# Kernel tuning notes

Measured on AMD Instinct MI355X. Metric: run time of the kernel, lower is better.

## Reference

```python
import jax, jax.numpy as jnp
import numpy as np

NUM_SCALES = 4
ENC = 64
KMAX = 16
DT = 0.005  # base_time_constant; original code's (undefined) self.dt interpreted as this


def setup_inputs() -> dict:
    key = jax.random.key(0)
    ks = jax.random.split(key, 5)
    events = jax.random.normal(ks[0], (2, 2, 32, 32, 64), dtype=jnp.float32)
    # matches torch.logspace(-3, -1, num_scales)
    time_constants = jnp.logspace(-3.0, -1.0, NUM_SCALES).astype(jnp.float32)
    temporal_kernels = jax.random.normal(ks[1], (NUM_SCALES, ENC, KMAX), dtype=jnp.float32)
    w1 = jax.random.normal(ks[2], (2 * NUM_SCALES, NUM_SCALES), dtype=jnp.float32) * 0.1
    b1 = jnp.zeros((2 * NUM_SCALES,), dtype=jnp.float32)
    w2 = jax.random.normal(ks[3], (NUM_SCALES, 2 * NUM_SCALES), dtype=jnp.float32) * 0.1
    b2 = jnp.zeros((NUM_SCALES,), dtype=jnp.float32)
    return {"events": events, "time_constants": time_constants,
            "temporal_kernels": temporal_kernels, "w1": w1, "b1": b1, "w2": w2, "b2": b2}


def reference(events, time_constants, temporal_kernels, w1, b1, w2, b2):
    B, C, H, W, T = events.shape
    k = min(KMAX, T)
    # decay kernels per scale: [S, k], normalized to sum 1
    t_idx = jnp.arange(k, dtype=jnp.float32)
    decay = jnp.exp(-t_idx[None, :] * DT / time_constants[:, None])
    decay = decay / decay.sum(axis=-1, keepdims=True)
    # combined learnable kernels: [S, E, k]
    combined = decay[:, None, :] * temporal_kernels[:, :, :k]

    Cf = C * H * W
    # one batched cross-correlation (torch F.conv1d semantics == lax conv, no flip)
    x = events.reshape(B * Cf, 1, T)                       # [B*Cf, 1, T]
    kern = combined.reshape(NUM_SCALES * ENC, 1, k)        # [S*E, 1, k]
    out = jax.lax.conv_general_dilated(
        x, kern, window_strides=(1,), padding=[(k // 2, k // 2)],
        dimension_numbers=("NCH", "OIH", "NCH"))           # [B*Cf, S*E, T+1]
    Tp = out.shape[-1]
    # [B, E, S, Cf, Tp] matching torch stack order (enc at dim1, scale at dim2)
    feats = out.reshape(B, Cf, NUM_SCALES, ENC, Tp).transpose(0, 3, 2, 1, 4)

    # torch .var() is unbiased -> ddof=1
    feature_variance = feats.var(axis=-1, ddof=1).mean(axis=(1, 3))  # [B, S]
    h = jax.nn.relu(feature_variance @ w1.T + b1)
    attn = jax.nn.softmax(h @ w2.T + b2, axis=-1)                    # [B, S]

    encoded = (feats * attn[:, None, :, None, None]).sum(axis=2)     # [B, E, Cf, Tp]
    return encoded
```

## Files before the change

kernel.cpp:

```cpp
#include <hip/hip_runtime.h>

#define KK 16
#define SS 4
#define EE 64
#define BB 2
#define DT_CONST 0.005f

typedef float f32x4 __attribute__((ext_vector_type(4)));
typedef short bf16x8 __attribute__((ext_vector_type(8)));

#define WS_WK_F 34816

__global__ void __launch_bounds__(512, 1) kA_gram(const float* __restrict__ events,
                                                  float* __restrict__ ws) {
    __shared__ float xs[16][97];
    __shared__ float S1L[16][16];
    __shared__ float part[16][136];
    const int tid = threadIdx.x;

    if (tid < 256) {
        const float4* src = reinterpret_cast<const float4*>(
            events + (size_t)blockIdx.x * 1024);
        float4 v = src[tid];
        int r = tid >> 4, c0 = ((tid & 15) << 2) + 8;
        xs[r][c0] = v.x; xs[r][c0+1] = v.y; xs[r][c0+2] = v.z; xs[r][c0+3] = v.w;
    }
    for (int idx = tid; idx < 16 * 33; idx += 512) {
        int rr = idx / 33, k = idx % 33;
        xs[rr][(k < 8) ? k : (k + 64)] = 0.f;
    }
    __syncthreads();

    const int r   = tid >> 5;
    const int c   = tid & 31;
    const int lag = c >> 1;
    const int h   = c & 1;
    const int off = h * 33;
    const float inv65 = 1.f / 65.f;

    {
        float s = 0.f;
#pragma unroll
        for (int j = 0; j < 32; ++j) s += xs[r][lag + off + j];
        if (!h) s += xs[r][lag + 32];
        s += __shfl_xor(s, 1, 64);
        if (!h) S1L[r][lag] = s;
    }
    __syncthreads();

    {
        float C = 0.f;
#pragma unroll
        for (int j = 0; j < 32; ++j) C += xs[r][off + j] * xs[r][off + j + lag];
        if (!h) C += xs[r][32] * xs[r][32 + lag];
        {
            float Ct = C + __shfl_xor(C, 1, 64);
            if (!h) part[r][lag] = Ct - S1L[r][0] * S1L[r][lag] * inv65;
        }
#pragma unroll
        for (int d1 = 1; d1 <= 15; ++d1) {
            const int add = d1 + off + 32 - h;
            const int rem = d1 - 1 + off;
            C += xs[r][add] * xs[r][add + lag] - xs[r][rem] * xs[r][rem + lag];
            if (lag + d1 <= 15) {
                float Ct = C + __shfl_xor(C, 1, 64);
                if (!h) {
                    int p = 16 * d1 - ((d1 * (d1 - 1)) >> 1) + lag;
                    part[r][p] = Ct - S1L[r][d1] * S1L[r][d1 + lag] * inv65;
                }
            } else {
            }
        }
    }
    __syncthreads();

    if (tid < 136) {
        float g = 0.f;
#pragma unroll
        for (int rr = 0; rr < 16; ++rr) g += part[rr][tid];
        ws[((size_t)((blockIdx.x >> 7) * 136 + tid)) * 128 + (blockIdx.x & 127)] = g;
    }
}

__global__ void __launch_bounds__(256, 1) kM_mlp(const float* __restrict__ tc,
        const float* __restrict__ tk, const float* __restrict__ w1,
        const float* __restrict__ b1, const float* __restrict__ w2,
        const float* __restrict__ b2, float* __restrict__ ws) {
    __shared__ float Gf[2 * 256];
    __shared__ float combL[SS * EE * KK];
    __shared__ float fvL[BB * SS];
    __shared__ float attnL[BB][SS];
    const int tid = threadIdx.x;

    for (int v = tid; v < 272; v += 256) {
        int b = (v >= 136) ? 1 : 0;
        int p = v - b * 136;
        int pp = p, d1 = 0;
        while (pp >= KK - d1) { pp -= KK - d1; ++d1; }
        int d2 = d1 + pp;
        const float4* rp = reinterpret_cast<const float4*>(ws + (size_t)v * 128);
        float acc = 0.f;
#pragma unroll
        for (int i = 0; i < 32; ++i) { float4 q = rp[i]; acc += (q.x + q.y) + (q.z + q.w); }
        Gf[b * 256 + d1 * KK + d2] = acc;
        Gf[b * 256 + d2 * KK + d1] = acc;
    }
    {
        int s = tid >> 6;
        float inv = DT_CONST / tc[s];
        float dk[KK]; float dsum = 0.f;
#pragma unroll
        for (int j = 0; j < KK; ++j) { dk[j] = expf(-(float)j * inv); dsum += dk[j]; }
        float rn = 1.f / dsum;
#pragma unroll
        for (int i = 0; i < 4; ++i) {
            float4 v = reinterpret_cast<const float4*>(tk + tid * KK)[i];
            combL[tid * KK + 4*i + 0] = dk[4*i + 0] * rn * v.x;
            combL[tid * KK + 4*i + 1] = dk[4*i + 1] * rn * v.y;
            combL[tid * KK + 4*i + 2] = dk[4*i + 2] * rn * v.z;
            combL[tid * KK + 4*i + 3] = dk[4*i + 3] * rn * v.w;
        }
    }
    __syncthreads();
    {
        float cvec[KK];
#pragma unroll
        for (int i = 0; i < 4; ++i) {
            float4 v = reinterpret_cast<const float4*>(combL + tid * KK)[i];
            cvec[4*i] = v.x; cvec[4*i+1] = v.y; cvec[4*i+2] = v.z; cvec[4*i+3] = v.w;
        }
        float acc0 = 0.f, acc1 = 0.f;
#pragma unroll
        for (int d1 = 0; d1 < KK; ++d1) {
            float cd1 = cvec[d1];
            float t0 = 0.5f * Gf[d1 * KK + d1] * cd1;
            float t1 = 0.5f * Gf[256 + d1 * KK + d1] * cd1;
#pragma unroll
            for (int d2 = d1 + 1; d2 < KK; ++d2) {
                t0 += Gf[d1 * KK + d2] * cvec[d2];
                t1 += Gf[256 + d1 * KK + d2] * cvec[d2];
            }
            acc0 += 2.f * cd1 * t0;
            acc1 += 2.f * cd1 * t1;
        }
#pragma unroll
        for (int sft = 1; sft < 64; sft <<= 1) {
            acc0 += __shfl_xor(acc0, sft, 64);
            acc1 += __shfl_xor(acc1, sft, 64);
        }
        if ((tid & 63) == 0) {
            const float scale = 1.f / 8388608.f;
            fvL[(tid >> 6)]     = acc0 * scale;
            fvL[4 + (tid >> 6)] = acc1 * scale;
        }
    }
    __syncthreads();
    if (tid < 2) {
        int b = tid;
        float h[8];
#pragma unroll
        for (int i = 0; i < 8; ++i) {
            float a = b1[i];
#pragma unroll
            for (int s = 0; s < SS; ++s) a += fvL[b * SS + s] * w1[i * SS + s];
            h[i] = a > 0.f ? a : 0.f;
        }
        float lg[SS]; float mx = -1e30f;
#pragma unroll
        for (int s = 0; s < SS; ++s) {
            float a = b2[s];
#pragma unroll
            for (int i = 0; i < 8; ++i) a += h[i] * w2[s * 8 + i];
            lg[s] = a; mx = fmaxf(mx, a);
        }
        float se = 0.f;
#pragma unroll
        for (int s = 0; s < SS; ++s) { lg[s] = expf(lg[s] - mx); se += lg[s]; }
#pragma unroll
        for (int s = 0; s < SS; ++s) attnL[b][s] = lg[s] / se;
    }
    __syncthreads();
    {
        unsigned short* wkp = reinterpret_cast<unsigned short*>(ws + WS_WK_F);
#pragma unroll
        for (int j = 0; j < 8; ++j) {
            int o = tid * 8 + j;
            int b = o >> 10, e = (o >> 4) & 63, k = o & 15;
            float a = 0.f;
#pragma unroll
            for (int s = 0; s < SS; ++s)
                a += attnL[b][s] * combL[(s * EE + e) * KK + k];
            unsigned int bits = __float_as_uint(a);
            unsigned short hh = (unsigned short)(bits >> 16);
            float hf = __uint_as_float(((unsigned int)hh) << 16);
            unsigned short ll = (unsigned short)(__float_as_uint(a - hf) >> 16);
            int base = b * 2048 + e * 32 + k;
            wkp[base]          = hh;   wkp[base + 16]        = 0;
            wkp[4096 + base]   = ll;   wkp[4096 + base + 16] = 0;
        }
    }
}

__global__ void __launch_bounds__(256, 8) kC_conv(const float* __restrict__ events,
                                                  const float* __restrict__ ws,
                                                  float* __restrict__ out) {
    __shared__ float xs[2][97];
    __shared__ __align__(16) unsigned short Bh[80 * 24 + 16];
    __shared__ __align__(16) unsigned short Bl[80 * 24 + 16];
    const int tid = threadIdx.x;
    const int bid = blockIdx.x;
    const int b   = bid >> 10;
    const int cf0 = (bid & 1023) << 1;
    const int w   = tid >> 6, l = tid & 63, llo = l & 15, lhi = l >> 4;

    for (int idx = tid; idx < 80 * 24 + 16; idx += 256) { Bh[idx] = 0; Bl[idx] = 0; }

    const unsigned short* wkp = reinterpret_cast<const unsigned short*>(ws + WS_WK_F);
    bf16x8 Ah = *reinterpret_cast<const bf16x8*>(wkp + b * 2048 + (w * 16 + llo) * 32 + 8 * lhi);
    bf16x8 Al = *reinterpret_cast<const bf16x8*>(wkp + 4096 + b * 2048 + (w * 16 + llo) * 32 + 8 * lhi);

    if (tid < 32) {
        float4 v = reinterpret_cast<const float4*>(
            events + ((size_t)b * 2048 + cf0) * 64)[tid];
        int rr = tid >> 4, c0 = ((tid & 15) << 2) + 8;
        xs[rr][c0] = v.x; xs[rr][c0+1] = v.y; xs[rr][c0+2] = v.z; xs[rr][c0+3] = v.w;
    }
    for (int idx = tid; idx < 66; idx += 256) {
        int rr = idx / 33, k = idx % 33;
        xs[rr][(k < 8) ? k : (k + 64)] = 0.f;
    }
    __syncthreads();

#pragma unroll 1
    for (int rr = 0; rr < 2; ++rr) {
#pragma unroll
        for (int q = 0; q < 5; ++q) {
            int idx = tid + q * 256;
            int t = idx >> 4, k = idx & 15;
            float x = xs[rr][t + k];
            unsigned int bits = __float_as_uint(x);
            unsigned short hh = (unsigned short)(bits >> 16);
            float hf = __uint_as_float(((unsigned int)hh) << 16);
            unsigned short ll = (unsigned short)(__float_as_uint(x - hf) >> 16);
            Bh[t * 24 + k] = hh;
            Bl[t * 24 + k] = ll;
        }
        __syncthreads();

        const size_t obase = ((size_t)(b * 64 + w * 16 + lhi * 4) * 2048 + (cf0 + rr)) * 65;
#pragma unroll
        for (int nt = 0; nt < 5; ++nt) {
            bf16x8 Xh = *reinterpret_cast<const bf16x8*>(Bh + (nt * 16 + llo) * 24 + 8 * lhi);
            bf16x8 Xl = *reinterpret_cast<const bf16x8*>(Bl + (nt * 16 + llo) * 24 + 8 * lhi);
            f32x4 acc = {0.f, 0.f, 0.f, 0.f};
            acc = __builtin_amdgcn_mfma_f32_16x16x32_bf16(Al, Xh, acc, 0, 0, 0);
            acc = __builtin_amdgcn_mfma_f32_16x16x32_bf16(Ah, Xl, acc, 0, 0, 0);
            acc = __builtin_amdgcn_mfma_f32_16x16x32_bf16(Ah, Xh, acc, 0, 0, 0);
            const int t0 = nt * 16 + llo;
            if (t0 < 65) {
#pragma unroll
                for (int i = 0; i < 4; ++i)
                    out[obase + (size_t)i * (2048 * 65) + t0] = acc[i];
            }
        }
        __syncthreads();
    }
}

extern "C" void kernel_launch(void* const* d_in, const int* in_sizes, int n_in,
                              void* d_out, int out_size, void* d_ws, size_t ws_size,
                              hipStream_t stream) {
    const float* events = (const float*)d_in[0];
    const float* tc     = (const float*)d_in[1];
    const float* tk     = (const float*)d_in[2];
    const float* w1     = (const float*)d_in[3];
    const float* b1     = (const float*)d_in[4];
    const float* w2     = (const float*)d_in[5];
    const float* b2     = (const float*)d_in[6];
    float* out = (float*)d_out;
    float* ws  = (float*)d_ws;

    hipLaunchKernelGGL(kA_gram, dim3(256),  dim3(512), 0, stream, events, ws);
    hipLaunchKernelGGL(kM_mlp,  dim3(1),    dim3(256), 0, stream, tc, tk, w1, b1, w2, b2, ws);
    hipLaunchKernelGGL(kC_conv, dim3(2048), dim3(256), 0, stream, events, ws, out);
}
```

Measured before the change: 37.95 us.

## Fuse attention MLP into conv kernel and reduce Gram partials with atomics

New measurement: 43.81 us. 1.15x slower.

```diff
diff --git a/kernel.cpp b/kernel.cpp
--- a/kernel.cpp
+++ b/kernel.cpp
@@ -9,7 +9,6 @@
 typedef float f32x4 __attribute__((ext_vector_type(4)));
 typedef short bf16x8 __attribute__((ext_vector_type(8)));
 
-#define WS_WK_F 34816
 
 __global__ void __launch_bounds__(512, 1) kA_gram(const float* __restrict__ events,
                                                   float* __restrict__ ws) {
@@ -68,7 +67,6 @@
                     int p = 16 * d1 - ((d1 * (d1 - 1)) >> 1) + lag;
                     part[r][p] = Ct - S1L[r][d1] * S1L[r][d1 + lag] * inv65;
                 }
-            } else {
             }
         }
     }
@@ -78,133 +76,22 @@
         float g = 0.f;
 #pragma unroll
         for (int rr = 0; rr < 16; ++rr) g += part[rr][tid];
-        ws[((size_t)((blockIdx.x >> 7) * 136 + tid)) * 128 + (blockIdx.x & 127)] = g;
+        atomicAdd(&ws[(blockIdx.x >> 7) * 136 + tid], g);
     }
 }
 
-__global__ void __launch_bounds__(256, 1) kM_mlp(const float* __restrict__ tc,
+__global__ void __launch_bounds__(256, 8) kC_conv(
+        const float* __restrict__ events, const float* __restrict__ tc,
         const float* __restrict__ tk, const float* __restrict__ w1,
         const float* __restrict__ b1, const float* __restrict__ w2,
-        const float* __restrict__ b2, float* __restrict__ ws) {
+        const float* __restrict__ b2, const float* __restrict__ ws,
+        float* __restrict__ out) {
+    __shared__ float xs[2][97];
     __shared__ float Gf[2 * 256];
-    __shared__ float combL[SS * EE * KK];
+    __shared__ float decayL[SS * KK];
     __shared__ float fvL[BB * SS];
-    __shared__ float attnL[BB][SS];
-    const int tid = threadIdx.x;
-
-    for (int v = tid; v < 272; v += 256) {
-        int b = (v >= 136) ? 1 : 0;
-        int p = v - b * 136;
-        int pp = p, d1 = 0;
-        while (pp >= KK - d1) { pp -= KK - d1; ++d1; }
-        int d2 = d1 + pp;
-        const float4* rp = reinterpret_cast<const float4*>(ws + (size_t)v * 128);
-        float acc = 0.f;
-#pragma unroll
-        for (int i = 0; i < 32; ++i) { float4 q = rp[i]; acc += (q.x + q.y) + (q.z + q.w); }
-        Gf[b * 256 + d1 * KK + d2] = acc;
-        Gf[b * 256 + d2 * KK + d1] = acc;
-    }
-    {
-        int s = tid >> 6;
-        float inv = DT_CONST / tc[s];
-        float dk[KK]; float dsum = 0.f;
-#pragma unroll
-        for (int j = 0; j < KK; ++j) { dk[j] = expf(-(float)j * inv); dsum += dk[j]; }
-        float rn = 1.f / dsum;
-#pragma unroll
-        for (int i = 0; i < 4; ++i) {
-            float4 v = reinterpret_cast<const float4*>(tk + tid * KK)[i];
-            combL[tid * KK + 4*i + 0] = dk[4*i + 0] * rn * v.x;
-            combL[tid * KK + 4*i + 1] = dk[4*i + 1] * rn * v.y;
-            combL[tid * KK + 4*i + 2] = dk[4*i + 2] * rn * v.z;
-            combL[tid * KK + 4*i + 3] = dk[4*i + 3] * rn * v.w;
-        }
-    }
-    __syncthreads();
-    {
-        float cvec[KK];
-#pragma unroll
-        for (int i = 0; i < 4; ++i) {
-            float4 v = reinterpret_cast<const float4*>(combL + tid * KK)[i];
-            cvec[4*i] = v.x; cvec[4*i+1] = v.y; cvec[4*i+2] = v.z; cvec[4*i+3] = v.w;
-        }
-        float acc0 = 0.f, acc1 = 0.f;
-#pragma unroll
-        for (int d1 = 0; d1 < KK; ++d1) {
-            float cd1 = cvec[d1];
-            float t0 = 0.5f * Gf[d1 * KK + d1] * cd1;
-            float t1 = 0.5f * Gf[256 + d1 * KK + d1] * cd1;
-#pragma unroll
-            for (int d2 = d1 + 1; d2 < KK; ++d2) {
-                t0 += Gf[d1 * KK + d2] * cvec[d2];
-                t1 += Gf[256 + d1 * KK + d2] * cvec[d2];
-            }
-            acc0 += 2.f * cd1 * t0;
-            acc1 += 2.f * cd1 * t1;
-        }
-#pragma unroll
-        for (int sft = 1; sft < 64; sft <<= 1) {
-            acc0 += __shfl_xor(acc0, sft, 64);
-            acc1 += __shfl_xor(acc1, sft, 64);
-        }
-        if ((tid & 63) == 0) {
-            const float scale = 1.f / 8388608.f;
-            fvL[(tid >> 6)]     = acc0 * scale;
-            fvL[4 + (tid >> 6)] = acc1 * scale;
-        }
-    }
-    __syncthreads();
-    if (tid < 2) {
-        int b = tid;
-        float h[8];
-#pragma unroll
-        for (int i = 0; i < 8; ++i) {
-            float a = b1[i];
-#pragma unroll
-            for (int s = 0; s < SS; ++s) a += fvL[b * SS + s] * w1[i * SS + s];
-            h[i] = a > 0.f ? a : 0.f;
-        }
-        float lg[SS]; float mx = -1e30f;
-#pragma unroll
-        for (int s = 0; s < SS; ++s) {
-            float a = b2[s];
-#pragma unroll
-            for (int i = 0; i < 8; ++i) a += h[i] * w2[s * 8 + i];
-            lg[s] = a; mx = fmaxf(mx, a);
-        }
-        float se = 0.f;
-#pragma unroll
-        for (int s = 0; s < SS; ++s) { lg[s] = expf(lg[s] - mx); se += lg[s]; }
-#pragma unroll
-        for (int s = 0; s < SS; ++s) attnL[b][s] = lg[s] / se;
-    }
-    __syncthreads();
-    {
-        unsigned short* wkp = reinterpret_cast<unsigned short*>(ws + WS_WK_F);
-#pragma unroll
-        for (int j = 0; j < 8; ++j) {
-            int o = tid * 8 + j;
-            int b = o >> 10, e = (o >> 4) & 63, k = o & 15;
-            float a = 0.f;
-#pragma unroll
-            for (int s = 0; s < SS; ++s)
-                a += attnL[b][s] * combL[(s * EE + e) * KK + k];
-            unsigned int bits = __float_as_uint(a);
-            unsigned short hh = (unsigned short)(bits >> 16);
-            float hf = __uint_as_float(((unsigned int)hh) << 16);
-            unsigned short ll = (unsigned short)(__float_as_uint(a - hf) >> 16);
-            int base = b * 2048 + e * 32 + k;
-            wkp[base]          = hh;   wkp[base + 16]        = 0;
-            wkp[4096 + base]   = ll;   wkp[4096 + base + 16] = 0;
-        }
-    }
-}
-
-__global__ void __launch_bounds__(256, 8) kC_conv(const float* __restrict__ events,
-                                                  const float* __restrict__ ws,
-                                                  float* __restrict__ out) {
-    __shared__ float xs[2][97];
+    __shared__ __align__(16) unsigned short wkh[64 * 32];
+    __shared__ __align__(16) unsigned short wkl[64 * 32];
     __shared__ __align__(16) unsigned short Bh[80 * 24 + 16];
     __shared__ __align__(16) unsigned short Bl[80 * 24 + 16];
     const int tid = threadIdx.x;
@@ -213,12 +100,8 @@
     const int cf0 = (bid & 1023) << 1;
     const int w   = tid >> 6, l = tid & 63, llo = l & 15, lhi = l >> 4;
 
+    for (int idx = tid; idx < 2048; idx += 256) { wkh[idx] = 0; wkl[idx] = 0; }
     for (int idx = tid; idx < 80 * 24 + 16; idx += 256) { Bh[idx] = 0; Bl[idx] = 0; }
-
-    const unsigned short* wkp = reinterpret_cast<const unsigned short*>(ws + WS_WK_F);
-    bf16x8 Ah = *reinterpret_cast<const bf16x8*>(wkp + b * 2048 + (w * 16 + llo) * 32 + 8 * lhi);
-    bf16x8 Al = *reinterpret_cast<const bf16x8*>(wkp + 4096 + b * 2048 + (w * 16 + llo) * 32 + 8 * lhi);
-
     if (tid < 32) {
         float4 v = reinterpret_cast<const float4*>(
             events + ((size_t)b * 2048 + cf0) * 64)[tid];
@@ -229,7 +112,120 @@
         int rr = idx / 33, k = idx % 33;
         xs[rr][(k < 8) ? k : (k + 64)] = 0.f;
     }
-    __syncthreads();
+    for (int v = tid; v < 272; v += 256) {
+        int b2i = (v >= 136) ? 1 : 0;
+        int p  = v - b2i * 136;
+        int pp = p, d1 = 0;
+        while (pp >= KK - d1) { pp -= KK - d1; ++d1; }
+        int d2 = d1 + pp;
+        float g = ws[v];
+        Gf[b2i * 256 + d1 * KK + d2] = g;
+        Gf[b2i * 256 + d2 * KK + d1] = g;
+    }
+    if (tid < SS) {
+        float inv = DT_CONST / tc[tid];
+        float d[KK]; float sum = 0.f;
+#pragma unroll
+        for (int k = 0; k < KK; ++k) { d[k] = expf(-(float)k * inv); sum += d[k]; }
+        float rn = 1.f / sum;
+#pragma unroll
+        for (int k = 0; k < KK; ++k) decayL[tid * KK + k] = d[k] * rn;
+    }
+    __syncthreads();
+
+    {
+        const int s = tid >> 6, e = tid & 63;
+        const float4* tkr = reinterpret_cast<const float4*>(tk + (s * EE + e) * KK);
+        float cvec[KK];
+#pragma unroll
+        for (int i = 0; i < 4; ++i) {
+            float4 v = tkr[i];
+            cvec[4*i+0] = decayL[s * KK + 4*i+0] * v.x;
+            cvec[4*i+1] = decayL[s * KK + 4*i+1] * v.y;
+            cvec[4*i+2] = decayL[s * KK + 4*i+2] * v.z;
+            cvec[4*i+3] = decayL[s * KK + 4*i+3] * v.w;
+        }
+        float acc0 = 0.f, acc1 = 0.f;
+#pragma unroll
+        for (int d1 = 0; d1 < KK; ++d1) {
+            float cd1 = cvec[d1];
+            float t0 = 0.5f * Gf[d1 * KK + d1] * cd1;
+            float t1 = 0.5f * Gf[256 + d1 * KK + d1] * cd1;
+#pragma unroll
+            for (int d2 = d1 + 1; d2 < KK; ++d2) {
+                t0 += Gf[d1 * KK + d2] * cvec[d2];
+                t1 += Gf[256 + d1 * KK + d2] * cvec[d2];
+            }
+            acc0 += 2.f * cd1 * t0;
+            acc1 += 2.f * cd1 * t1;
+        }
+#pragma unroll
+        for (int sft = 1; sft < 64; sft <<= 1) {
+            acc0 += __shfl_xor(acc0, sft, 64);
+            acc1 += __shfl_xor(acc1, sft, 64);
+        }
+        if ((tid & 63) == 0) {
+            const float scale = 1.f / 8388608.f;
+            fvL[s]     = acc0 * scale;
+            fvL[4 + s] = acc1 * scale;
+        }
+    }
+    __syncthreads();
+
+    {
+        float fv[SS];
+#pragma unroll
+        for (int s = 0; s < SS; ++s) fv[s] = fvL[b * SS + s];
+        float h[8];
+#pragma unroll
+        for (int i = 0; i < 8; ++i) {
+            float a = b1[i];
+#pragma unroll
+            for (int s = 0; s < SS; ++s) a += fv[s] * w1[i * SS + s];
+            h[i] = a > 0.f ? a : 0.f;
+        }
+        float lg[SS]; float mx = -1e30f;
+#pragma unroll
+        for (int s = 0; s < SS; ++s) {
+            float a = b2[s];
+#pragma unroll
+            for (int i = 0; i < 8; ++i) a += h[i] * w2[s * 8 + i];
+            lg[s] = a; mx = fmaxf(mx, a);
+        }
+        float se = 0.f;
+#pragma unroll
+        for (int s = 0; s < SS; ++s) { lg[s] = expf(lg[s] - mx); se += lg[s]; }
+        float attn[SS];
+#pragma unroll
+        for (int s = 0; s < SS; ++s) attn[s] = lg[s] / se;
+
+        const int o4 = tid * 4;
+        const int e  = o4 >> 4, k0 = o4 & 15;
+        float vj0 = 0.f, vj1 = 0.f, vj2 = 0.f, vj3 = 0.f;
+#pragma unroll
+        for (int s = 0; s < SS; ++s) {
+            float4 tv = *reinterpret_cast<const float4*>(tk + (s * EE + e) * KK + k0);
+            float as = attn[s];
+            vj0 += as * decayL[s * KK + k0 + 0] * tv.x;
+            vj1 += as * decayL[s * KK + k0 + 1] * tv.y;
+            vj2 += as * decayL[s * KK + k0 + 2] * tv.z;
+            vj3 += as * decayL[s * KK + k0 + 3] * tv.w;
+        }
+        float vv[4] = {vj0, vj1, vj2, vj3};
+#pragma unroll
+        for (int j = 0; j < 4; ++j) {
+            unsigned int bits = __float_as_uint(vv[j]);
+            unsigned short hh = (unsigned short)(bits >> 16);
+            float hf = __uint_as_float(((unsigned int)hh) << 16);
+            unsigned short ll = (unsigned short)(__float_as_uint(vv[j] - hf) >> 16);
+            wkh[e * 32 + k0 + j] = hh;
+            wkl[e * 32 + k0 + j] = ll;
+        }
+    }
+    __syncthreads();
+
+    bf16x8 Ah = *reinterpret_cast<const bf16x8*>(&wkh[(w * 16 + llo) * 32 + 8 * lhi]);
+    bf16x8 Al = *reinterpret_cast<const bf16x8*>(&wkl[(w * 16 + llo) * 32 + 8 * lhi]);
 
 #pragma unroll 1
     for (int rr = 0; rr < 2; ++rr) {
@@ -280,7 +276,8 @@
     float* out = (float*)d_out;
     float* ws  = (float*)d_ws;
 
+    hipMemsetAsync(ws, 0, 272 * sizeof(float), stream);
     hipLaunchKernelGGL(kA_gram, dim3(256),  dim3(512), 0, stream, events, ws);
-    hipLaunchKernelGGL(kM_mlp,  dim3(1),    dim3(256), 0, stream, tc, tk, w1, b1, w2, b2, ws);
-    hipLaunchKernelGGL(kC_conv, dim3(2048), dim3(256), 0, stream, events, ws, out);
+    hipLaunchKernelGGL(kC_conv, dim3(2048), dim3(256), 0, stream,
+                       events, tc, tk, w1, b1, w2, b2, ws, out);
 }
```
